# Kernel tuning notes

Measured on AMD Instinct MI355X. Metric: run time of the kernel, lower is better.

The kernel has to match this reference:

```python
import jax, jax.numpy as jnp
import numpy as np

B, N1, N2, D = 4, 4096, 4096, 128


def setup_inputs() -> dict:
    key = jax.random.key(0)
    k1, k2 = jax.random.split(key)
    x1 = jax.random.normal(k1, (B, N1, D), dtype=jnp.float32)
    x2 = jax.random.normal(k2, (B, N2, D), dtype=jnp.float32)
    return {"x1": x1, "x2": x2}


def reference(x1, x2):
    # torch.cdist(x2, x1, p=2.0): pairwise euclidean distances [B, N2, N1]
    # Expansion form: ||a||^2 + ||b||^2 - 2 a.b  (single GEMM, no [B,N2,N1,D] intermediate)
    sq2 = jnp.sum(x2 * x2, axis=-1)                      # [B, N2]
    sq1 = jnp.sum(x1 * x1, axis=-1)                      # [B, N1]
    inner = jnp.einsum('bnd,bmd->bnm', x2, x1)           # [B, N2, N1]
    sq = sq2[:, :, None] + sq1[:, None, :] - 2.0 * inner
    corr_mat = jnp.sqrt(jnp.maximum(sq, 0.0))            # clamp numerical negatives
    max_ind21 = jnp.argmin(corr_mat, axis=-1)            # [B, N2] nearest x1 for each x2
    max_ind12 = jnp.argmin(corr_mat, axis=-2)            # [B, N1] nearest x2 for each x1
    return (x1, x2, corr_mat, max_ind12, max_ind21)
```

## Files before the change

kernel.cpp:

```cpp
#include <hip/hip_runtime.h>
#include <stdint.h>
#include <stddef.h>

#define BB 4
#define NN 4096
#define DD 128

typedef _Float16 f16;
typedef _Float16 f16x8 __attribute__((ext_vector_type(8)));
typedef float f32x4 __attribute__((ext_vector_type(4)));

__device__ __forceinline__ void gl16(const f16* g, f16* l) {
  __builtin_amdgcn_global_load_lds(
      (const __attribute__((address_space(1))) unsigned int*)g,
      (__attribute__((address_space(3))) unsigned int*)l,
      16, 0, 0);
}

__global__ __launch_bounds__(256) void prep_kernel(
    const float* __restrict__ x1, const float* __restrict__ x2,
    f16* __restrict__ x1h, f16* __restrict__ x1l,
    f16* __restrict__ x2h, f16* __restrict__ x2l,
    float* __restrict__ sq1, float* __restrict__ sq2,
    float* __restrict__ out)
{
  int gtid = blockIdx.x * blockDim.x + threadIdx.x;
  int gwave = gtid >> 6;
  int lane = gtid & 63;
  int sub = lane >> 3;
  int j = lane & 7;
  int row = gwave * 8 + sub;
  const float* src; f16* dh; f16* dl; float* sq; float* cpy; int r;
  if (row < BB * NN) {
    r = row; src = x1; dh = x1h; dl = x1l; sq = sq1; cpy = out;
  } else {
    r = row - BB * NN; src = x2; dh = x2h; dl = x2l; sq = sq2;
    cpy = out + (size_t)BB * NN * DD;
  }
  const float* p = src + (size_t)r * DD;
  float acc = 0.0f;
  #pragma unroll
  for (int i = 0; i < DD / 8; ++i) {
    int c = j + i * 8;
    float v = p[c];
    float s = v * v;
    acc = (i == 0) ? s : (acc + s);
    f16 h = (f16)v;
    f16 l = (f16)(v - (float)h);
    dh[(size_t)r * DD + c] = h;
    dl[(size_t)r * DD + c] = l;
    cpy[(size_t)r * DD + c] = v;
  }
  acc = acc + __shfl_xor(acc, 1);
  acc = acc + __shfl_xor(acc, 2);
  acc = acc + __shfl_xor(acc, 4);
  if (j == 0) sq[r] = acc;
}

__global__ __launch_bounds__(256) void cdist_kernel(
    const f16* __restrict__ x1h, const f16* __restrict__ x1l,
    const f16* __restrict__ x2h, const f16* __restrict__ x2l,
    const float* __restrict__ sq1, const float* __restrict__ sq2,
    float* __restrict__ corr,
    float* __restrict__ p21v, int* __restrict__ p21i,
    float* __restrict__ p12v, int* __restrict__ p12i)
{
  __shared__ f16 Ah[128 * 32];
  __shared__ f16 Al[128 * 32];
  __shared__ f16 Bh[128 * 32];
  __shared__ f16 Bl[128 * 32];
  __shared__ float s1s[128];
  __shared__ float s2s[128];

  const int b = blockIdx.z;
  const int bn1 = blockIdx.x * 128;
  const int bn2 = blockIdx.y * 128;
  const int t = threadIdx.x;
  const int wid = t >> 6;
  const int lane = t & 63;
  const int wm = wid >> 1;
  const int wn = wid & 1;
  const int lr = lane & 15;
  const int lg = lane >> 4;

  const f16* gAh = x1h + (size_t)b * NN * DD;
  const f16* gAl = x1l + (size_t)b * NN * DD;
  const f16* gBh = x2h + (size_t)b * NN * DD;
  const f16* gBl = x2l + (size_t)b * NN * DD;

  if (t < 128) s1s[t] = sq1[(size_t)b * NN + bn1 + t];
  else         s2s[t - 128] = sq2[(size_t)b * NN + bn2 + (t - 128)];

  int goff_[2], loff_[2];
  #pragma unroll
  for (int i = 0; i < 2; ++i) {
    const int c = wid * 128 + i * 64 + lane;
    const int rowc = c >> 2;
    const int kc = (c & 3) ^ (rowc & 3) ^ ((rowc >> 2) & 3);
    goff_[i] = rowc * DD + kc * 8;
    loff_[i] = (wid * 128 + i * 64) * 8;
  }
#define STAGE(k0) do { \
    _Pragma("unroll") \
    for (int i = 0; i < 2; ++i) { \
      gl16(gAh + (bn1 * DD + goff_[i] + (k0)), &Ah[loff_[i]]); \
      gl16(gAl + (bn1 * DD + goff_[i] + (k0)), &Al[loff_[i]]); \
      gl16(gBh + (bn2 * DD + goff_[i] + (k0)), &Bh[loff_[i]]); \
      gl16(gBl + (bn2 * DD + goff_[i] + (k0)), &Bl[loff_[i]]); \
    } } while (0)

  f32x4 acc[4][4];
  #pragma unroll
  for (int m = 0; m < 4; ++m)
    #pragma unroll
    for (int n = 0; n < 4; ++n)
      #pragma unroll
      for (int q = 0; q < 4; ++q) acc[m][n][q] = 0.0f;

  STAGE(0);

  const int lgx8 = (lg ^ (lr & 3) ^ ((lr >> 2) & 3)) * 8;
  const int offA0 = (wm * 64 + lr) * 32 + lgx8;
  const int offB0 = (wn * 64 + lr) * 32 + lgx8;

  for (int it = 0; it < 4; ++it) {
    __syncthreads();
    f16x8 fah[4], fal[4], fbh[4], fbl[4];
    #pragma unroll
    for (int m = 0; m < 4; ++m) {
      const int off = offA0 + m * (16 * 32);
      fah[m] = *(const f16x8*)&Ah[off];
      fal[m] = *(const f16x8*)&Al[off];
    }
    #pragma unroll
    for (int n = 0; n < 4; ++n) {
      const int off = offB0 + n * (16 * 32);
      fbh[n] = *(const f16x8*)&Bh[off];
      fbl[n] = *(const f16x8*)&Bl[off];
    }
    __syncthreads();
    if (it < 3) STAGE((it + 1) * 32);
    #pragma unroll
    for (int m = 0; m < 4; ++m)
      #pragma unroll
      for (int n = 0; n < 4; ++n) {
        acc[m][n] = __builtin_amdgcn_mfma_f32_16x16x32_f16(fah[m], fbh[n], acc[m][n], 0, 0, 0);
        acc[m][n] = __builtin_amdgcn_mfma_f32_16x16x32_f16(fah[m], fbl[n], acc[m][n], 0, 0, 0);
        acc[m][n] = __builtin_amdgcn_mfma_f32_16x16x32_f16(fal[m], fbh[n], acc[m][n], 0, 0, 0);
      }
  }
#undef STAGE

  float s2r[4];
  #pragma unroll
  for (int n = 0; n < 4; ++n) s2r[n] = s2s[wn * 64 + n * 16 + lr];
  float s1r[4][4];
  #pragma unroll
  for (int m = 0; m < 4; ++m)
    #pragma unroll
    for (int q = 0; q < 4; ++q) s1r[m][q] = s1s[wm * 64 + m * 16 + lg * 4 + q];

  float v21[4]; int i21[4];
  #pragma unroll
  for (int n = 0; n < 4; ++n) { v21[n] = 3.4e38f; i21[n] = 0; }

  float* cbp = corr + (size_t)b * NN * NN;
  #pragma unroll
  for (int m = 0; m < 4; ++m) {
    const int n1b = wm * 64 + m * 16 + lg * 4;
    float v12[4]; int i12[4];
    #pragma unroll
    for (int q = 0; q < 4; ++q) { v12[q] = 3.4e38f; i12[q] = 0; }
    #pragma unroll
    for (int n = 0; n < 4; ++n) {
      const int n2l = wn * 64 + n * 16 + lr;
      f32x4 dv;
      float sqc[4];
      #pragma unroll
      for (int q = 0; q < 4; ++q) {
        const float sv = fmaxf(fmaf(-2.0f, acc[m][n][q], s1r[m][q] + s2r[n]), 0.0f);
        sqc[q] = sv;
        dv[q] = sqrtf(sv);
      }
      *(f32x4*)(cbp + (size_t)(bn2 + n2l) * NN + (bn1 + n1b)) = dv;
      #pragma unroll
      for (int q = 0; q < 4; ++q) {
        if (sqc[q] < v21[n]) { v21[n] = sqc[q]; i21[n] = bn1 + n1b + q; }
        if (sqc[q] < v12[q]) { v12[q] = sqc[q]; i12[q] = bn2 + n2l; }
      }
    }
    #pragma unroll
    for (int q = 0; q < 4; ++q) {
      float v = v12[q]; int idx = i12[q];
      #pragma unroll
      for (int mask = 1; mask < 16; mask <<= 1) {
        float ov = __shfl_xor(v, mask);
        int oi = __shfl_xor(idx, mask);
        if (ov < v || (ov == v && oi < idx)) { v = ov; idx = oi; }
      }
      if (lr == 0) {
        const int colg = bn1 + n1b + q;
        const size_t o = ((size_t)b * NN + colg) * 64 + (blockIdx.y * 2 + wn);
        p12v[o] = v; p12i[o] = idx;
      }
    }
  }
  #pragma unroll
  for (int n = 0; n < 4; ++n) {
    float v = v21[n]; int idx = i21[n];
    #pragma unroll
    for (int mask = 16; mask < 64; mask <<= 1) {
      float ov = __shfl_xor(v, mask);
      int oi = __shfl_xor(idx, mask);
      if (ov < v || (ov == v && oi < idx)) { v = ov; idx = oi; }
    }
    if (lg == 0) {
      const int rowg = bn2 + wn * 64 + n * 16 + lr;
      const size_t o = ((size_t)b * NN + rowg) * 64 + (blockIdx.x * 2 + wm);
      p21v[o] = v; p21i[o] = idx;
    }
  }
}

__global__ __launch_bounds__(256) void argmin_reduce_kernel(
    const float* __restrict__ p21v, const int* __restrict__ p21i,
    const float* __restrict__ p12v, const int* __restrict__ p12i,
    float* __restrict__ out_i12, float* __restrict__ out_i21)
{
  int gtid = blockIdx.x * blockDim.x + threadIdx.x;
  int gwave = gtid >> 6;
  int lane = gtid & 63;
  const float* pv; const int* pi; float* dst; int r;
  if (gwave < BB * NN) { r = gwave; pv = p21v; pi = p21i; dst = out_i21; }
  else { r = gwave - BB * NN; pv = p12v; pi = p12i; dst = out_i12; }
  float v = pv[(size_t)r * 64 + lane];
  int idx = pi[(size_t)r * 64 + lane];
  #pragma unroll
  for (int mask = 1; mask < 64; mask <<= 1) {
    float ov = __shfl_xor(v, mask);
    int oi = __shfl_xor(idx, mask);
    if (ov < v || (ov == v && oi < idx)) { v = ov; idx = oi; }
  }
  if (lane == 0) dst[r] = (float)idx;
}

extern "C" void kernel_launch(void* const* d_in, const int* in_sizes, int n_in,
                              void* d_out, int out_size, void* d_ws, size_t ws_size,
                              hipStream_t stream) {
  (void)in_sizes; (void)n_in; (void)out_size; (void)ws_size;
  const float* x1 = (const float*)d_in[0];
  const float* x2 = (const float*)d_in[1];
  float* out = (float*)d_out;
  char* ws = (char*)d_ws;
  const size_t nd = (size_t)BB * NN * DD;

  f16* x1h = (f16*)(ws + 0 * nd * 2);
  f16* x1l = (f16*)(ws + 1 * nd * 2);
  f16* x2h = (f16*)(ws + 2 * nd * 2);
  f16* x2l = (f16*)(ws + 3 * nd * 2);
  float* sq1 = (float*)(ws + 4 * nd * 2);
  float* sq2 = (float*)(ws + 4 * nd * 2 + (size_t)BB * NN * 4);
  char* pbase = ws + 4 * nd * 2 + 2 * (size_t)BB * NN * 4;
  float* p21v = (float*)(pbase + 0 * (size_t)BB * NN * 64 * 4);
  int*   p21i = (int*)  (pbase + 1 * (size_t)BB * NN * 64 * 4);
  float* p12v = (float*)(pbase + 2 * (size_t)BB * NN * 64 * 4);
  int*   p12i = (int*)  (pbase + 3 * (size_t)BB * NN * 64 * 4);

  hipLaunchKernelGGL(prep_kernel, dim3(1024), dim3(256), 0, stream,
                     x1, x2, x1h, x1l, x2h, x2l, sq1, sq2, out);

  float* corr = out + 2 * nd;
  hipLaunchKernelGGL(cdist_kernel, dim3(32, 32, 4), dim3(256), 0, stream,
                     x1h, x1l, x2h, x2l, sq1, sq2, corr, p21v, p21i, p12v, p12i);

  float* out_i12 = out + 2 * nd + (size_t)BB * NN * NN;
  float* out_i21 = out_i12 + (size_t)BB * NN;
  hipLaunchKernelGGL(argmin_reduce_kernel, dim3(8192), dim3(256), 0, stream,
                     p21v, p21i, p12v, p12i, out_i12, out_i21);
}
```

Before: 179.8 us.

## Use 512-thread blocks with smaller per-wave tiles, swizzled block order, fast sqrt

Each cdist block now runs 8 waves instead of 4. Every wave computes a 64x32 sub-tile, which halves its accumulators and raises occupancy, and each thread issues one global-to-LDS load per buffer instead of two. The block index is remapped in groups of 8 to improve L2 reuse. The distance store becomes non-temporal, sqrt uses a raw v_sqrt_f32, and the p12 partial buffer widens to 128 slots per column, which the reduce kernel folds in with one extra comparison. The costs are more shuffle-reduction work per block and raw-instruction sqrt precision that may differ slightly from IEEE sqrtf.

New measurement: 152.2 us. 1.18x faster.

```diff
diff --git a/kernel.cpp b/kernel.cpp
--- a/kernel.cpp
+++ b/kernel.cpp
@@ -15,6 +15,12 @@
       (const __attribute__((address_space(1))) unsigned int*)g,
       (__attribute__((address_space(3))) unsigned int*)l,
       16, 0, 0);
+}
+
+__device__ __forceinline__ float fast_sqrt(float x) {
+  float r;
+  asm("v_sqrt_f32 %0, %1" : "=v"(r) : "v"(x));
+  return r;
 }
 
 __global__ __launch_bounds__(256) void prep_kernel(
@@ -57,7 +63,7 @@
   if (j == 0) sq[r] = acc;
 }
 
-__global__ __launch_bounds__(256) void cdist_kernel(
+__global__ __launch_bounds__(512, 4) void cdist_kernel(
     const f16* __restrict__ x1h, const f16* __restrict__ x1l,
     const f16* __restrict__ x2h, const f16* __restrict__ x2l,
     const float* __restrict__ sq1, const float* __restrict__ sq2,
@@ -73,13 +79,18 @@
   __shared__ float s2s[128];
 
   const int b = blockIdx.z;
-  const int bn1 = blockIdx.x * 128;
-  const int bn2 = blockIdx.y * 128;
+  int lin = blockIdx.y * 32 + blockIdx.x;
+  lin = (lin & 7) * 128 + (lin >> 3);
+  const int sbx = lin & 31;
+  const int sby = lin >> 5;
+  const int bn1 = sbx * 128;
+  const int bn2 = sby * 128;
+
   const int t = threadIdx.x;
   const int wid = t >> 6;
   const int lane = t & 63;
-  const int wm = wid >> 1;
-  const int wn = wid & 1;
+  const int wm = wid & 1;
+  const int wn = wid >> 1;
   const int lr = lane & 15;
   const int lg = lane >> 4;
 
@@ -89,31 +100,24 @@
   const f16* gBl = x2l + (size_t)b * NN * DD;
 
   if (t < 128) s1s[t] = sq1[(size_t)b * NN + bn1 + t];
-  else         s2s[t - 128] = sq2[(size_t)b * NN + bn2 + (t - 128)];
-
-  int goff_[2], loff_[2];
-  #pragma unroll
-  for (int i = 0; i < 2; ++i) {
-    const int c = wid * 128 + i * 64 + lane;
-    const int rowc = c >> 2;
-    const int kc = (c & 3) ^ (rowc & 3) ^ ((rowc >> 2) & 3);
-    goff_[i] = rowc * DD + kc * 8;
-    loff_[i] = (wid * 128 + i * 64) * 8;
-  }
+  else if (t < 256) s2s[t - 128] = sq2[(size_t)b * NN + bn2 + (t - 128)];
+
+  const int rowc = t >> 2;
+  const int kc = (t & 3) ^ (rowc & 3) ^ ((rowc >> 2) & 3);
+  const int aoff = bn1 * DD + rowc * DD + kc * 8;
+  const int boff = bn2 * DD + rowc * DD + kc * 8;
+  const int loff = (wid * 64) * 8;
 #define STAGE(k0) do { \
-    _Pragma("unroll") \
-    for (int i = 0; i < 2; ++i) { \
-      gl16(gAh + (bn1 * DD + goff_[i] + (k0)), &Ah[loff_[i]]); \
-      gl16(gAl + (bn1 * DD + goff_[i] + (k0)), &Al[loff_[i]]); \
-      gl16(gBh + (bn2 * DD + goff_[i] + (k0)), &Bh[loff_[i]]); \
-      gl16(gBl + (bn2 * DD + goff_[i] + (k0)), &Bl[loff_[i]]); \
-    } } while (0)
-
-  f32x4 acc[4][4];
+    gl16(gAh + aoff + (k0), &Ah[loff]); \
+    gl16(gAl + aoff + (k0), &Al[loff]); \
+    gl16(gBh + boff + (k0), &Bh[loff]); \
+    gl16(gBl + boff + (k0), &Bl[loff]); } while (0)
+
+  f32x4 acc[4][2];
   #pragma unroll
   for (int m = 0; m < 4; ++m)
     #pragma unroll
-    for (int n = 0; n < 4; ++n)
+    for (int n = 0; n < 2; ++n)
       #pragma unroll
       for (int q = 0; q < 4; ++q) acc[m][n][q] = 0.0f;
 
@@ -121,29 +125,27 @@
 
   const int lgx8 = (lg ^ (lr & 3) ^ ((lr >> 2) & 3)) * 8;
   const int offA0 = (wm * 64 + lr) * 32 + lgx8;
-  const int offB0 = (wn * 64 + lr) * 32 + lgx8;
+  const int offB0 = (wn * 32 + lr) * 32 + lgx8;
 
   for (int it = 0; it < 4; ++it) {
     __syncthreads();
-    f16x8 fah[4], fal[4], fbh[4], fbl[4];
+    f16x8 fah[4], fal[4], fbh[2], fbl[2];
     #pragma unroll
     for (int m = 0; m < 4; ++m) {
-      const int off = offA0 + m * (16 * 32);
-      fah[m] = *(const f16x8*)&Ah[off];
-      fal[m] = *(const f16x8*)&Al[off];
-    }
-    #pragma unroll
-    for (int n = 0; n < 4; ++n) {
-      const int off = offB0 + n * (16 * 32);
-      fbh[n] = *(const f16x8*)&Bh[off];
-      fbl[n] = *(const f16x8*)&Bl[off];
+      fah[m] = *(const f16x8*)&Ah[offA0 + m * 512];
+      fal[m] = *(const f16x8*)&Al[offA0 + m * 512];
+    }
+    #pragma unroll
+    for (int n = 0; n < 2; ++n) {
+      fbh[n] = *(const f16x8*)&Bh[offB0 + n * 512];
+      fbl[n] = *(const f16x8*)&Bl[offB0 + n * 512];
     }
     __syncthreads();
     if (it < 3) STAGE((it + 1) * 32);
     #pragma unroll
     for (int m = 0; m < 4; ++m)
       #pragma unroll
-      for (int n = 0; n < 4; ++n) {
+      for (int n = 0; n < 2; ++n) {
         acc[m][n] = __builtin_amdgcn_mfma_f32_16x16x32_f16(fah[m], fbh[n], acc[m][n], 0, 0, 0);
         acc[m][n] = __builtin_amdgcn_mfma_f32_16x16x32_f16(fah[m], fbl[n], acc[m][n], 0, 0, 0);
         acc[m][n] = __builtin_amdgcn_mfma_f32_16x16x32_f16(fal[m], fbh[n], acc[m][n], 0, 0, 0);
@@ -151,18 +153,18 @@
   }
 #undef STAGE
 
-  float s2r[4];
-  #pragma unroll
-  for (int n = 0; n < 4; ++n) s2r[n] = s2s[wn * 64 + n * 16 + lr];
+  float s2r[2];
+  #pragma unroll
+  for (int n = 0; n < 2; ++n) s2r[n] = s2s[wn * 32 + n * 16 + lr];
   float s1r[4][4];
   #pragma unroll
   for (int m = 0; m < 4; ++m)
     #pragma unroll
     for (int q = 0; q < 4; ++q) s1r[m][q] = s1s[wm * 64 + m * 16 + lg * 4 + q];
 
-  float v21[4]; int i21[4];
-  #pragma unroll
-  for (int n = 0; n < 4; ++n) { v21[n] = 3.4e38f; i21[n] = 0; }
+  float v21[2]; int i21[2];
+  #pragma unroll
+  for (int n = 0; n < 2; ++n) { v21[n] = 3.4e38f; i21[n] = 0; }
 
   float* cbp = corr + (size_t)b * NN * NN;
   #pragma unroll
@@ -172,17 +174,17 @@
     #pragma unroll
     for (int q = 0; q < 4; ++q) { v12[q] = 3.4e38f; i12[q] = 0; }
     #pragma unroll
-    for (int n = 0; n < 4; ++n) {
-      const int n2l = wn * 64 + n * 16 + lr;
+    for (int n = 0; n < 2; ++n) {
+      const int n2l = wn * 32 + n * 16 + lr;
       f32x4 dv;
       float sqc[4];
       #pragma unroll
       for (int q = 0; q < 4; ++q) {
         const float sv = fmaxf(fmaf(-2.0f, acc[m][n][q], s1r[m][q] + s2r[n]), 0.0f);
         sqc[q] = sv;
-        dv[q] = sqrtf(sv);
-      }
-      *(f32x4*)(cbp + (size_t)(bn2 + n2l) * NN + (bn1 + n1b)) = dv;
+        dv[q] = fast_sqrt(sv);
+      }
+      __builtin_nontemporal_store(dv, (f32x4*)(cbp + (size_t)(bn2 + n2l) * NN + (bn1 + n1b)));
       #pragma unroll
       for (int q = 0; q < 4; ++q) {
         if (sqc[q] < v21[n]) { v21[n] = sqc[q]; i21[n] = bn1 + n1b + q; }
@@ -200,13 +202,13 @@
       }
       if (lr == 0) {
         const int colg = bn1 + n1b + q;
-        const size_t o = ((size_t)b * NN + colg) * 64 + (blockIdx.y * 2 + wn);
+        const size_t o = ((size_t)b * NN + colg) * 128 + (sby * 4 + wn);
         p12v[o] = v; p12i[o] = idx;
       }
     }
   }
   #pragma unroll
-  for (int n = 0; n < 4; ++n) {
+  for (int n = 0; n < 2; ++n) {
     float v = v21[n]; int idx = i21[n];
     #pragma unroll
     for (int mask = 16; mask < 64; mask <<= 1) {
@@ -215,8 +217,8 @@
       if (ov < v || (ov == v && oi < idx)) { v = ov; idx = oi; }
     }
     if (lg == 0) {
-      const int rowg = bn2 + wn * 64 + n * 16 + lr;
-      const size_t o = ((size_t)b * NN + rowg) * 64 + (blockIdx.x * 2 + wm);
+      const int rowg = bn2 + wn * 32 + n * 16 + lr;
+      const size_t o = ((size_t)b * NN + rowg) * 64 + (sbx * 2 + wm);
       p21v[o] = v; p21i[o] = idx;
     }
   }
@@ -230,11 +232,21 @@
   int gtid = blockIdx.x * blockDim.x + threadIdx.x;
   int gwave = gtid >> 6;
   int lane = gtid & 63;
-  const float* pv; const int* pi; float* dst; int r;
-  if (gwave < BB * NN) { r = gwave; pv = p21v; pi = p21i; dst = out_i21; }
-  else { r = gwave - BB * NN; pv = p12v; pi = p12i; dst = out_i12; }
-  float v = pv[(size_t)r * 64 + lane];
-  int idx = pi[(size_t)r * 64 + lane];
+  float v; int idx; float* dst; int r;
+  if (gwave < BB * NN) {
+    r = gwave;
+    v = p21v[(size_t)r * 64 + lane];
+    idx = p21i[(size_t)r * 64 + lane];
+    dst = out_i21;
+  } else {
+    r = gwave - BB * NN;
+    v = p12v[(size_t)r * 128 + lane];
+    idx = p12i[(size_t)r * 128 + lane];
+    float v2 = p12v[(size_t)r * 128 + 64 + lane];
+    int i2 = p12i[(size_t)r * 128 + 64 + lane];
+    if (v2 < v || (v2 == v && i2 < idx)) { v = v2; idx = i2; }
+    dst = out_i12;
+  }
   #pragma unroll
   for (int mask = 1; mask < 64; mask <<= 1) {
     float ov = __shfl_xor(v, mask);
@@ -253,28 +265,29 @@
   float* out = (float*)d_out;
   char* ws = (char*)d_ws;
   const size_t nd = (size_t)BB * NN * DD;
+  const size_t bn = (size_t)BB * NN;
 
   f16* x1h = (f16*)(ws + 0 * nd * 2);
   f16* x1l = (f16*)(ws + 1 * nd * 2);
   f16* x2h = (f16*)(ws + 2 * nd * 2);
   f16* x2l = (f16*)(ws + 3 * nd * 2);
   float* sq1 = (float*)(ws + 4 * nd * 2);
-  float* sq2 = (float*)(ws + 4 * nd * 2 + (size_t)BB * NN * 4);
-  char* pbase = ws + 4 * nd * 2 + 2 * (size_t)BB * NN * 4;
-  float* p21v = (float*)(pbase + 0 * (size_t)BB * NN * 64 * 4);
-  int*   p21i = (int*)  (pbase + 1 * (size_t)BB * NN * 64 * 4);
-  float* p12v = (float*)(pbase + 2 * (size_t)BB * NN * 64 * 4);
-  int*   p12i = (int*)  (pbase + 3 * (size_t)BB * NN * 64 * 4);
+  float* sq2 = (float*)(ws + 4 * nd * 2 + bn * 4);
+  char* pbase = ws + 4 * nd * 2 + 2 * bn * 4;
+  float* p21v = (float*)(pbase);
+  int*   p21i = (int*)  (pbase + 1 * bn * 64 * 4);
+  float* p12v = (float*)(pbase + 2 * bn * 64 * 4);
+  int*   p12i = (int*)  (pbase + 2 * bn * 64 * 4 + bn * 128 * 4);
 
   hipLaunchKernelGGL(prep_kernel, dim3(1024), dim3(256), 0, stream,
                      x1, x2, x1h, x1l, x2h, x2l, sq1, sq2, out);
 
   float* corr = out + 2 * nd;
-  hipLaunchKernelGGL(cdist_kernel, dim3(32, 32, 4), dim3(256), 0, stream,
+  hipLaunchKernelGGL(cdist_kernel, dim3(32, 32, 4), dim3(512), 0, stream,
                      x1h, x1l, x2h, x2l, sq1, sq2, corr, p21v, p21i, p12v, p12i);
 
-  float* out_i12 = out + 2 * nd + (size_t)BB * NN * NN;
-  float* out_i21 = out_i12 + (size_t)BB * NN;
+  float* out_i12 = out + 2 * nd + bn * (size_t)NN;
+  float* out_i21 = out_i12 + bn;
   hipLaunchKernelGGL(argmin_reduce_kernel, dim3(8192), dim3(256), 0, stream,
                      p21v, p21i, p12v, p12i, out_i12, out_i21);
 }
```

## Load MFMA operands directly from global memory and remap blocks for L2 locality

Applied to the files above, without the earlier changes.

Removes the shared-memory staging and block barriers from the cdist kernel. Each wave now loads its f16 hi/lo fragments straight from global memory into registers, and the block tile becomes 64 x 256 with one 64x64 sub-tile per wave. Block indices are swizzled for L2 reuse, occupancy is hinted at 3 blocks per SIMD, the sqrt uses the raw v_sqrt_f32 instruction, and the distance matrix is written with nontemporal stores. This drops LDS traffic and sync overhead, at the cost of redundant global/L2 reads of the x1 rows across waves and no prefetch overlap between loads and MFMA.

Result: slower. 189.5 us (+5.4%).

```diff
diff --git a/kernel.cpp b/kernel.cpp
--- a/kernel.cpp
+++ b/kernel.cpp
@@ -10,11 +10,10 @@
 typedef _Float16 f16x8 __attribute__((ext_vector_type(8)));
 typedef float f32x4 __attribute__((ext_vector_type(4)));
 
-__device__ __forceinline__ void gl16(const f16* g, f16* l) {
-  __builtin_amdgcn_global_load_lds(
-      (const __attribute__((address_space(1))) unsigned int*)g,
-      (__attribute__((address_space(3))) unsigned int*)l,
-      16, 0, 0);
+__device__ __forceinline__ float fast_sqrt(float x) {
+  float r;
+  asm("v_sqrt_f32 %0, %1" : "=v"(r) : "v"(x));
+  return r;
 }
 
 __global__ __launch_bounds__(256) void prep_kernel(
@@ -57,7 +56,7 @@
   if (j == 0) sq[r] = acc;
 }
 
-__global__ __launch_bounds__(256) void cdist_kernel(
+__global__ __launch_bounds__(256, 3) void cdist_kernel(
     const f16* __restrict__ x1h, const f16* __restrict__ x1l,
     const f16* __restrict__ x2h, const f16* __restrict__ x2l,
     const float* __restrict__ sq1, const float* __restrict__ sq2,
@@ -65,49 +64,31 @@
     float* __restrict__ p21v, int* __restrict__ p21i,
     float* __restrict__ p12v, int* __restrict__ p12i)
 {
-  __shared__ f16 Ah[128 * 32];
-  __shared__ f16 Al[128 * 32];
-  __shared__ f16 Bh[128 * 32];
-  __shared__ f16 Bl[128 * 32];
-  __shared__ float s1s[128];
-  __shared__ float s2s[128];
-
   const int b = blockIdx.z;
-  const int bn1 = blockIdx.x * 128;
-  const int bn2 = blockIdx.y * 128;
+  int lin = blockIdx.y * 64 + blockIdx.x;
+  lin = (lin & 7) * 128 + (lin >> 3);
+  const int sbx = lin & 63;
+  const int sby = lin >> 6;
+  const int bn1 = sbx * 64;
+
   const int t = threadIdx.x;
-  const int wid = t >> 6;
+  const int w = t >> 6;
   const int lane = t & 63;
-  const int wm = wid >> 1;
-  const int wn = wid & 1;
   const int lr = lane & 15;
   const int lg = lane >> 4;
-
-  const f16* gAh = x1h + (size_t)b * NN * DD;
-  const f16* gAl = x1l + (size_t)b * NN * DD;
-  const f16* gBh = x2h + (size_t)b * NN * DD;
-  const f16* gBl = x2l + (size_t)b * NN * DD;
-
-  if (t < 128) s1s[t] = sq1[(size_t)b * NN + bn1 + t];
-  else         s2s[t - 128] = sq2[(size_t)b * NN + bn2 + (t - 128)];
-
-  int goff_[2], loff_[2];
-  #pragma unroll
-  for (int i = 0; i < 2; ++i) {
-    const int c = wid * 128 + i * 64 + lane;
-    const int rowc = c >> 2;
-    const int kc = (c & 3) ^ (rowc & 3) ^ ((rowc >> 2) & 3);
-    goff_[i] = rowc * DD + kc * 8;
-    loff_[i] = (wid * 128 + i * 64) * 8;
-  }
-#define STAGE(k0) do { \
-    _Pragma("unroll") \
-    for (int i = 0; i < 2; ++i) { \
-      gl16(gAh + (bn1 * DD + goff_[i] + (k0)), &Ah[loff_[i]]); \
-      gl16(gAl + (bn1 * DD + goff_[i] + (k0)), &Al[loff_[i]]); \
-      gl16(gBh + (bn2 * DD + goff_[i] + (k0)), &Bh[loff_[i]]); \
-      gl16(gBl + (bn2 * DD + goff_[i] + (k0)), &Bl[loff_[i]]); \
-    } } while (0)
+  const int bn2 = sby * 256 + w * 64;
+
+  const size_t base = (size_t)b * NN * DD;
+  const f16* gAh = x1h + base;
+  const f16* gAl = x1l + base;
+  const f16* gBh = x2h + base;
+  const f16* gBl = x2l + base;
+
+  int voffA[4], voffB[4];
+  #pragma unroll
+  for (int m = 0; m < 4; ++m) voffA[m] = (bn1 + m * 16 + lr) * DD + lg * 8;
+  #pragma unroll
+  for (int n = 0; n < 4; ++n) voffB[n] = (bn2 + n * 16 + lr) * DD + lg * 8;
 
   f32x4 acc[4][4];
   #pragma unroll
@@ -117,48 +98,40 @@
       #pragma unroll
       for (int q = 0; q < 4; ++q) acc[m][n][q] = 0.0f;
 
-  STAGE(0);
-
-  const int lgx8 = (lg ^ (lr & 3) ^ ((lr >> 2) & 3)) * 8;
-  const int offA0 = (wm * 64 + lr) * 32 + lgx8;
-  const int offB0 = (wn * 64 + lr) * 32 + lgx8;
-
+  #pragma unroll
   for (int it = 0; it < 4; ++it) {
-    __syncthreads();
-    f16x8 fah[4], fal[4], fbh[4], fbl[4];
+    const int ko = it * 32;
+    f16x8 ah[4], al[4], bh[4], bl[4];
     #pragma unroll
     for (int m = 0; m < 4; ++m) {
-      const int off = offA0 + m * (16 * 32);
-      fah[m] = *(const f16x8*)&Ah[off];
-      fal[m] = *(const f16x8*)&Al[off];
+      ah[m] = *(const f16x8*)(gAh + voffA[m] + ko);
+      al[m] = *(const f16x8*)(gAl + voffA[m] + ko);
     }
     #pragma unroll
     for (int n = 0; n < 4; ++n) {
-      const int off = offB0 + n * (16 * 32);
-      fbh[n] = *(const f16x8*)&Bh[off];
-      fbl[n] = *(const f16x8*)&Bl[off];
-    }
-    __syncthreads();
-    if (it < 3) STAGE((it + 1) * 32);
-    #pragma unroll
-    for (int m = 0; m < 4; ++m)
-      #pragma unroll
-      for (int n = 0; n < 4; ++n) {
-        acc[m][n] = __builtin_amdgcn_mfma_f32_16x16x32_f16(fah[m], fbh[n], acc[m][n], 0, 0, 0);
-        acc[m][n] = __builtin_amdgcn_mfma_f32_16x16x32_f16(fah[m], fbl[n], acc[m][n], 0, 0, 0);
-        acc[m][n] = __builtin_amdgcn_mfma_f32_16x16x32_f16(fal[m], fbh[n], acc[m][n], 0, 0, 0);
-      }
-  }
-#undef STAGE
-
+      bh[n] = *(const f16x8*)(gBh + voffB[n] + ko);
+      bl[n] = *(const f16x8*)(gBl + voffB[n] + ko);
+    }
+    #pragma unroll
+    for (int n = 0; n < 4; ++n)
+      #pragma unroll
+      for (int m = 0; m < 4; ++m) {
+        acc[m][n] = __builtin_amdgcn_mfma_f32_16x16x32_f16(ah[m], bh[n], acc[m][n], 0, 0, 0);
+        acc[m][n] = __builtin_amdgcn_mfma_f32_16x16x32_f16(ah[m], bl[n], acc[m][n], 0, 0, 0);
+        acc[m][n] = __builtin_amdgcn_mfma_f32_16x16x32_f16(al[m], bh[n], acc[m][n], 0, 0, 0);
+      }
+  }
+
+  const float* sq1b = sq1 + (size_t)b * NN;
+  const float* sq2b = sq2 + (size_t)b * NN;
+  float s1r[4][4];
+  #pragma unroll
+  for (int m = 0; m < 4; ++m)
+    #pragma unroll
+    for (int q = 0; q < 4; ++q) s1r[m][q] = sq1b[bn1 + m * 16 + lg * 4 + q];
   float s2r[4];
   #pragma unroll
-  for (int n = 0; n < 4; ++n) s2r[n] = s2s[wn * 64 + n * 16 + lr];
-  float s1r[4][4];
-  #pragma unroll
-  for (int m = 0; m < 4; ++m)
-    #pragma unroll
-    for (int q = 0; q < 4; ++q) s1r[m][q] = s1s[wm * 64 + m * 16 + lg * 4 + q];
+  for (int n = 0; n < 4; ++n) s2r[n] = sq2b[bn2 + n * 16 + lr];
 
   float v21[4]; int i21[4];
   #pragma unroll
@@ -167,26 +140,26 @@
   float* cbp = corr + (size_t)b * NN * NN;
   #pragma unroll
   for (int m = 0; m < 4; ++m) {
-    const int n1b = wm * 64 + m * 16 + lg * 4;
+    const int n1b = bn1 + m * 16 + lg * 4;
     float v12[4]; int i12[4];
     #pragma unroll
     for (int q = 0; q < 4; ++q) { v12[q] = 3.4e38f; i12[q] = 0; }
     #pragma unroll
     for (int n = 0; n < 4; ++n) {
-      const int n2l = wn * 64 + n * 16 + lr;
+      const int n2g = bn2 + n * 16 + lr;
       f32x4 dv;
       float sqc[4];
       #pragma unroll
       for (int q = 0; q < 4; ++q) {
         const float sv = fmaxf(fmaf(-2.0f, acc[m][n][q], s1r[m][q] + s2r[n]), 0.0f);
         sqc[q] = sv;
-        dv[q] = sqrtf(sv);
-      }
-      *(f32x4*)(cbp + (size_t)(bn2 + n2l) * NN + (bn1 + n1b)) = dv;
+        dv[q] = fast_sqrt(sv);
+      }
+      __builtin_nontemporal_store(dv, (f32x4*)(cbp + (size_t)n2g * NN + n1b));
       #pragma unroll
       for (int q = 0; q < 4; ++q) {
-        if (sqc[q] < v21[n]) { v21[n] = sqc[q]; i21[n] = bn1 + n1b + q; }
-        if (sqc[q] < v12[q]) { v12[q] = sqc[q]; i12[q] = bn2 + n2l; }
+        if (sqc[q] < v21[n]) { v21[n] = sqc[q]; i21[n] = n1b + q; }
+        if (sqc[q] < v12[q]) { v12[q] = sqc[q]; i12[q] = n2g; }
       }
     }
     #pragma unroll
@@ -199,8 +172,7 @@
         if (ov < v || (ov == v && oi < idx)) { v = ov; idx = oi; }
       }
       if (lr == 0) {
-        const int colg = bn1 + n1b + q;
-        const size_t o = ((size_t)b * NN + colg) * 64 + (blockIdx.y * 2 + wn);
+        const size_t o = ((size_t)b * NN + n1b + q) * 64 + (sby * 4 + w);
         p12v[o] = v; p12i[o] = idx;
       }
     }
@@ -215,8 +187,7 @@
       if (ov < v || (ov == v && oi < idx)) { v = ov; idx = oi; }
     }
     if (lg == 0) {
-      const int rowg = bn2 + wn * 64 + n * 16 + lr;
-      const size_t o = ((size_t)b * NN + rowg) * 64 + (blockIdx.x * 2 + wm);
+      const size_t o = ((size_t)b * NN + bn2 + n * 16 + lr) * 64 + sbx;
       p21v[o] = v; p21i[o] = idx;
     }
   }
@@ -253,28 +224,29 @@
   float* out = (float*)d_out;
   char* ws = (char*)d_ws;
   const size_t nd = (size_t)BB * NN * DD;
+  const size_t bn = (size_t)BB * NN;
 
   f16* x1h = (f16*)(ws + 0 * nd * 2);
   f16* x1l = (f16*)(ws + 1 * nd * 2);
   f16* x2h = (f16*)(ws + 2 * nd * 2);
   f16* x2l = (f16*)(ws + 3 * nd * 2);
   float* sq1 = (float*)(ws + 4 * nd * 2);
-  float* sq2 = (float*)(ws + 4 * nd * 2 + (size_t)BB * NN * 4);
-  char* pbase = ws + 4 * nd * 2 + 2 * (size_t)BB * NN * 4;
-  float* p21v = (float*)(pbase + 0 * (size_t)BB * NN * 64 * 4);
-  int*   p21i = (int*)  (pbase + 1 * (size_t)BB * NN * 64 * 4);
-  float* p12v = (float*)(pbase + 2 * (size_t)BB * NN * 64 * 4);
-  int*   p12i = (int*)  (pbase + 3 * (size_t)BB * NN * 64 * 4);
+  float* sq2 = (float*)(ws + 4 * nd * 2 + bn * 4);
+  char* pbase = ws + 4 * nd * 2 + 2 * bn * 4;
+  float* p21v = (float*)(pbase + 0 * bn * 64 * 4);
+  int*   p21i = (int*)  (pbase + 1 * bn * 64 * 4);
+  float* p12v = (float*)(pbase + 2 * bn * 64 * 4);
+  int*   p12i = (int*)  (pbase + 3 * bn * 64 * 4);
 
   hipLaunchKernelGGL(prep_kernel, dim3(1024), dim3(256), 0, stream,
                      x1, x2, x1h, x1l, x2h, x2l, sq1, sq2, out);
 
   float* corr = out + 2 * nd;
-  hipLaunchKernelGGL(cdist_kernel, dim3(32, 32, 4), dim3(256), 0, stream,
+  hipLaunchKernelGGL(cdist_kernel, dim3(64, 16, 4), dim3(256), 0, stream,
                      x1h, x1l, x2h, x2l, sq1, sq2, corr, p21v, p21i, p12v, p12i);
 
-  float* out_i12 = out + 2 * nd + (size_t)BB * NN * NN;
-  float* out_i21 = out_i12 + (size_t)BB * NN;
+  float* out_i12 = out + 2 * nd + bn * (size_t)NN;
+  float* out_i21 = out_i12 + bn;
   hipLaunchKernelGGL(argmin_reduce_kernel, dim3(8192), dim3(256), 0, stream,
                      p21v, p21i, p12v, p12i, out_i12, out_i21);
 }
```
